# Performance work log

Hardware: AMD Instinct MI355X
Metric: run time of the kernel (lower is better)

## Reference

```python
import jax, jax.numpy as jnp
import numpy as np

V = 6890          # SMPL vertex count
RAYS, POINTS = 256, 64
LATENT_DIM = 16
RES_HI, RES_LO = 10, 4


def posenc(x, res):
    # NeRF-style encoding: [x, sin(2^k x), cos(2^k x)] for k in 0..res-1 -> D*(1+2*res)
    freqs = 2.0 ** jnp.arange(res, dtype=x.dtype)            # [res]
    xf = x[..., None, :] * freqs[:, None]                    # [..., res, D]
    n = x.shape[:-1]
    s = jnp.sin(xf).reshape(*n, -1)
    c = jnp.cos(xf).reshape(*n, -1)
    return jnp.concatenate([x, s, c], axis=-1)


def setup_inputs() -> dict:
    key = jax.random.key(0)
    ks = jax.random.split(key, 12)
    inp = {}
    inp['pts'] = jax.random.normal(ks[0], (RAYS, POINTS, 6), jnp.float32)
    inp['keypoints'] = jax.random.normal(ks[1], (V, 3), jnp.float32)
    # invertible per-vertex 4x4 transforms: identity + small noise, stored [4,4,V]
    noise = 0.1 * jax.random.normal(ks[2], (4, 4, V), jnp.float32)
    inp['trans_kp'] = jnp.eye(4, dtype=jnp.float32)[:, :, None] + noise
    inp['neighbors'] = jax.random.randint(ks[3], (V, 7), 0, V, jnp.int32)
    inp['rest_pose'] = jax.random.normal(ks[4], (V, 3), jnp.float32)
    inp['latent'] = jax.random.normal(ks[5], (V, LATENT_DIM), jnp.float32)
    d_in = 7 * ((2 * RES_HI + 1) * 4 + LATENT_DIM)  # 700
    inp['W1'] = 0.05 * jax.random.normal(ks[6], (d_in, 256), jnp.float32)
    inp['b1'] = jnp.zeros((256,), jnp.float32)
    inp['W2'] = 0.05 * jax.random.normal(ks[7], (256, 256), jnp.float32)
    inp['b2'] = jnp.zeros((256,), jnp.float32)
    inp['W3'] = 0.05 * jax.random.normal(ks[8], (256, 256), jnp.float32)
    inp['b3'] = jnp.zeros((256,), jnp.float32)
    return inp


def reference(pts, keypoints, trans_kp, neighbors, rest_pose, latent,
              W1, b1, W2, b2, W3, b3):
    rays, points, _ = pts.shape
    p, view_dir = jnp.split(pts, 2, axis=-1)
    p = p.reshape(rays * points, 3)                          # [N,3]

    # brute-force 1-NN of p into keypoints
    d2 = ((p * p).sum(-1, keepdims=True)
          - 2.0 * p @ keypoints.T
          + (keypoints * keypoints).sum(-1))                 # [N,V]
    knn_index = jnp.argmin(d2, axis=1)                       # [N]

    # inverse transforms, keep rotation part: [3,3,V]
    T = jnp.linalg.inv(jnp.transpose(trans_kp, (2, 0, 1)))   # [V,4,4]
    R = jnp.transpose(T, (1, 2, 0))[:3, :3]                  # [3,3,V]

    vidx = neighbors[knn_index]                              # [N,7]
    vdist = p[:, None, :] - keypoints[vidx]                  # [N,7,3]

    diff = p - keypoints[knn_index]                          # [N,3]
    Rg = R[:, :, knn_index]                                  # [3,3,N]
    direction = jnp.einsum('ijn,nj->ni', Rg, diff)           # [N,3]
    nrm = jnp.linalg.norm(direction, axis=-1, keepdims=True)
    direction = direction / jnp.maximum(nrm, 1e-12)

    vfeat = jnp.concatenate(
        [rest_pose[vidx].reshape(-1, 21),
         jnp.linalg.norm(vdist, axis=-1)], axis=-1)          # [N,28]
    lfeat = latent[vidx].reshape(-1, 7 * latent.shape[1])    # [N,112]

    h = jnp.concatenate([posenc(vfeat, RES_HI), lfeat], -1)  # [N,700]
    h = jax.nn.relu(h @ W1 + b1)
    h = jax.nn.relu(h @ W2 + b2)
    h = h @ W3 + b3                                          # [N,256]

    out = jnp.concatenate([h, posenc(direction, RES_LO)], -1)  # [N,283]
    return out.reshape(rays, points, -1)
```

## Files before the change

### kernel.cpp

```cpp
#include <hip/hip_runtime.h>
#include <hip/hip_bf16.h>
#include <math.h>

#define V_N   6890
#define N_PTS 16384
#define D_IN  700
#define D_INP 704
#define D_HID 256
#define D_OUT 283
#define NCHUNK 32
#define CHUNK  216
#define GAP_EPS 1e-4f

#define RINV4_OFF 0
#define KP4_OFF   82688
#define RP4_OFF   110272
#define PB4_OFF   170640
#define WT1_OFF   2267792
#define WT2_OFF   2357904
#define WT3_OFF   2390672
#define X_OFF     2423440

typedef __attribute__((ext_vector_type(8))) short short8;
typedef __attribute__((ext_vector_type(4))) float f32x4;

__device__ __forceinline__ unsigned short f2bf(float f) {
    unsigned int u = __builtin_bit_cast(unsigned int, f);
    u += 0x7fffu + ((u >> 16) & 1u);
    return (unsigned short)(u >> 16);
}

__device__ __forceinline__ float fsin(float x) {
    return __builtin_amdgcn_sinf(__builtin_amdgcn_fractf(x * 0.15915494309189535f));
}
__device__ __forceinline__ float fcos(float x) {
    return __builtin_amdgcn_cosf(__builtin_amdgcn_fractf(x * 0.15915494309189535f));
}

__device__ __forceinline__ void glds16(const void* g, void* l) {
    __builtin_amdgcn_global_load_lds(
        (const __attribute__((address_space(1))) void*)g,
        (__attribute__((address_space(3))) void*)l, 16, 0, 0);
}

__device__ __forceinline__ int swzoff(int r, int sub) {
    return ((r << 2) | (sub ^ ((r >> 1) & 3))) << 4;
}

__device__ __forceinline__ int rescan64(const float* __restrict__ pts,
                                        const float4* __restrict__ kp4,
                                        int nn, int lane) {
    double pxd = (double)pts[nn*6+0], pyd = (double)pts[nn*6+1], pzd = (double)pts[nn*6+2];
    double ppd = pxd*pxd + pyd*pyd + pzd*pzd;
    double best = 1e300; int bbi = 0x7fffffff;
    for (int jj = lane; jj < V_N; jj += 64) {
        float4 k = kp4[jj];
        double kx = (double)k.x, ky = (double)k.y, kz = (double)k.z;
        double d = ppd - 2.0*(pxd*kx + pyd*ky + pzd*kz) + (kx*kx + ky*ky + kz*kz);
        if (d < best || (d == best && jj < bbi)) { best = d; bbi = jj; }
    }
#pragma unroll
    for (int off = 32; off >= 1; off >>= 1) {
        double od = __shfl_xor(best, off);
        int    oi = __shfl_xor(bbi, off);
        if (od < best || (od == best && oi < bbi)) { best = od; bbi = oi; }
    }
    return bbi;
}

#define SCAN_BLOCKS 2048
#define PREP_BLOCKS 27
__global__ __launch_bounds__(256) void prep_scan_kernel(
    const float* __restrict__ pts, const float* __restrict__ keyp,
    const float* __restrict__ trans, const float* __restrict__ restp,
    const float* __restrict__ W1, const float* __restrict__ W2,
    const float* __restrict__ W3,
    float4* __restrict__ rinv4, float4* __restrict__ kp4, float4* __restrict__ rp4,
    unsigned short* __restrict__ wt1, unsigned short* __restrict__ wt2,
    unsigned short* __restrict__ wt3, float4* __restrict__ pb4)
{
    __shared__ float4 s_kp[CHUNK];
    int bx = blockIdx.x, tid = threadIdx.x;

    if (bx < SCAN_BLOCKS) {
        int c = bx >> 6;
        int n = (bx & 63) * 256 + tid;
        int v0 = c * CHUNK;
        int nv = min(V_N - v0, CHUNK);
        if (tid < nv) {
            int v = v0 + tid;
            float kx = keyp[v*3+0], ky = keyp[v*3+1], kz = keyp[v*3+2];
            s_kp[tid] = make_float4(kx, ky, kz, kx*kx + ky*ky + kz*kz);
        }
        __syncthreads();

        float px2n = -2.0f * pts[n*6+0], py2n = -2.0f * pts[n*6+1], pz2n = -2.0f * pts[n*6+2];
        float m1 = 1e30f, m2 = 1e30f;
        int bi = 0x7fffffff;

#define KNN_STEP(kk, jj)                                                    \
    {                                                                       \
        float d = __builtin_fmaf(px2n, kk.x,                                \
                  __builtin_fmaf(py2n, kk.y,                                \
                  __builtin_fmaf(pz2n, kk.z, kk.w)));                       \
        bool lt = d < m1;                                                   \
        bi = lt ? (jj) : bi;                                                \
        m2 = __builtin_amdgcn_fmed3f(m1, m2, d);                            \
        m1 = fminf(m1, d);                                                  \
    }
        int j = 0;
        for (; j + 8 <= nv; j += 8) {
            float4 k0 = s_kp[j],   k1 = s_kp[j+1], k2 = s_kp[j+2], k3 = s_kp[j+3];
            float4 k4 = s_kp[j+4], k5 = s_kp[j+5], k6 = s_kp[j+6], k7 = s_kp[j+7];
            KNN_STEP(k0, v0+j);   KNN_STEP(k1, v0+j+1);
            KNN_STEP(k2, v0+j+2); KNN_STEP(k3, v0+j+3);
            KNN_STEP(k4, v0+j+4); KNN_STEP(k5, v0+j+5);
            KNN_STEP(k6, v0+j+6); KNN_STEP(k7, v0+j+7);
        }
        for (; j < nv; ++j) {
            float4 k0 = s_kp[j];
            KNN_STEP(k0, v0+j);
        }
#undef KNN_STEP
        pb4[(size_t)n * NCHUNK + c] = make_float4(m1, m2, __int_as_float(bi), 0.0f);

    } else if (bx < SCAN_BLOCKS + PREP_BLOCKS) {
        int v = (bx - SCAN_BLOCKS) * 256 + tid;
        if (v >= V_N) return;
        float m[16];
#pragma unroll
        for (int i = 0; i < 16; ++i) m[i] = trans[i * V_N + v];

        float i0  =  m[5]*m[10]*m[15] - m[5]*m[11]*m[14] - m[9]*m[6]*m[15] + m[9]*m[7]*m[14] + m[13]*m[6]*m[11] - m[13]*m[7]*m[10];
        float i4  = -m[4]*m[10]*m[15] + m[4]*m[11]*m[14] + m[8]*m[6]*m[15] - m[8]*m[7]*m[14] - m[12]*m[6]*m[11] + m[12]*m[7]*m[10];
        float i8  =  m[4]*m[9]*m[15]  - m[4]*m[11]*m[13] - m[8]*m[5]*m[15] + m[8]*m[7]*m[13] + m[12]*m[5]*m[11] - m[12]*m[7]*m[9];
        float i12 = -m[4]*m[9]*m[14]  + m[4]*m[10]*m[13] + m[8]*m[5]*m[14] - m[8]*m[6]*m[13] - m[12]*m[5]*m[10] + m[12]*m[6]*m[9];
        float i1  = -m[1]*m[10]*m[15] + m[1]*m[11]*m[14] + m[9]*m[2]*m[15] - m[9]*m[3]*m[14] - m[13]*m[2]*m[11] + m[13]*m[3]*m[10];
        float i5  =  m[0]*m[10]*m[15] - m[0]*m[11]*m[14] - m[8]*m[2]*m[15] + m[8]*m[3]*m[14] + m[12]*m[2]*m[11] - m[12]*m[3]*m[10];
        float i9  = -m[0]*m[9]*m[15]  + m[0]*m[11]*m[13] + m[8]*m[1]*m[15] - m[8]*m[3]*m[13] - m[12]*m[1]*m[11] + m[12]*m[3]*m[9];
        float i2  =  m[1]*m[6]*m[15]  - m[1]*m[7]*m[14]  - m[5]*m[2]*m[15] + m[5]*m[3]*m[14] + m[13]*m[2]*m[7]  - m[13]*m[3]*m[6];
        float i6  = -m[0]*m[6]*m[15]  + m[0]*m[7]*m[14]  + m[4]*m[2]*m[15] - m[4]*m[3]*m[14] - m[12]*m[2]*m[7]  + m[12]*m[3]*m[6];
        float i10 =  m[0]*m[5]*m[15]  - m[0]*m[7]*m[13]  - m[4]*m[1]*m[15] + m[4]*m[3]*m[13] + m[12]*m[1]*m[7]  - m[12]*m[3]*m[5];

        float det = m[0]*i0 + m[1]*i4 + m[2]*i8 + m[3]*i12;
        float id = 1.0f / det;
        rinv4[v*3+0] = make_float4(i0*id, i1*id, i2*id, i4*id);
        rinv4[v*3+1] = make_float4(i5*id, i6*id, i8*id, i9*id);
        rinv4[v*3+2] = make_float4(i10*id, 0.0f, 0.0f, 0.0f);

        float kx = keyp[v*3], ky = keyp[v*3+1], kz = keyp[v*3+2];
        kp4[v] = make_float4(kx, ky, kz, kx*kx + ky*ky + kz*kz);
        rp4[v] = make_float4(restp[v*3], restp[v*3+1], restp[v*3+2], 0.0f);
    } else {
        int idx = (bx - SCAN_BLOCKS - PREP_BLOCKS) * 256 + tid;
        const int N1 = 256 * D_INP;
        const int N2 = 256 * 256;
        if (idx < N1) {
            int n = idx / D_INP, k = idx - n * D_INP;
            float v = (k < D_IN) ? W1[k * 256 + n] : 0.0f;
            wt1[n * D_INP + k] = f2bf(v);
        } else if (idx < N1 + N2) {
            int t = idx - N1;
            int n = t >> 8, k = t & 255;
            wt2[n * 256 + k] = f2bf(W2[k * 256 + n]);
        } else if (idx < N1 + 2 * N2) {
            int t = idx - N1 - N2;
            int n = t >> 8, k = t & 255;
            wt3[n * 256 + k] = f2bf(W3[k * 256 + n]);
        }
    }
}

__global__ __launch_bounds__(256) void feat_kernel(
    const float* __restrict__ pts, const int* __restrict__ neigh,
    const float* __restrict__ latent, const float4* __restrict__ rinv4,
    const float4* __restrict__ kp4, const float4* __restrict__ rp4,
    const float4* __restrict__ pb4, unsigned short* __restrict__ X,
    float* __restrict__ out)
{
    __shared__ float s_vf[4][2][29];
    __shared__ float s_dir[4][2][4];

    int t = threadIdx.x;
    int w = t >> 6, lane = t & 63;
    int n0 = blockIdx.x * 8 + w * 2;
    int ph = lane >> 5, g = lane & 31;

    float pxA = pts[n0*6+0],     pyA = pts[n0*6+1],     pzA = pts[n0*6+2];
    float pxB = pts[(n0+1)*6+0], pyB = pts[(n0+1)*6+1], pzB = pts[(n0+1)*6+2];

    float4 P = pb4[(size_t)(n0 + ph) * NCHUNK + g];
    float m1 = P.x, m2 = P.y;
    int   bi = __float_as_int(P.z);
#pragma unroll
    for (int off = 1; off <= 16; off <<= 1) {
        float o1 = __shfl_xor(m1, off);
        float o2 = __shfl_xor(m2, off);
        int   ob = __shfl_xor(bi, off);
        float nm2 = fminf(fminf(m2, o2), fmaxf(m1, o1));
        bool take = (o1 < m1) || (o1 == m1 && ob < bi);
        bi = take ? ob : bi;
        m1 = fminf(m1, o1);
        m2 = nm2;
    }
    unsigned long long ambmask = __ballot(m2 - m1 < GAP_EPS);
    if (ambmask & 1ull) {
        int r = rescan64(pts, kp4, n0, lane);
        if (ph == 0) bi = r;
    }
    if (ambmask & (1ull << 32)) {
        int r = rescan64(pts, kp4, n0 + 1, lane);
        if (ph == 1) bi = r;
    }

    int p = ph, j = g;
    int k8 = bi;
    float px = p ? pxB : pxA, py = p ? pyB : pyA, pz = p ? pzB : pzA;

    int v7 = 0;
    if (j < 7) {
        v7 = neigh[k8*7 + j];
        float4 kq = kp4[v7];
        float4 rq = rp4[v7];
        float dx = px - kq.x, dy = py - kq.y, dz = pz - kq.z;
        s_vf[w][p][j*3+0] = rq.x;
        s_vf[w][p][j*3+1] = rq.y;
        s_vf[w][p][j*3+2] = rq.z;
        s_vf[w][p][21+j]  = sqrtf(dx*dx + dy*dy + dz*dz);
    } else if (j == 7) {
        float4 kq = kp4[k8];
        float ddx = px - kq.x, ddy = py - kq.y, ddz = pz - kq.z;
        float4 R0 = rinv4[k8*3+0];
        float4 R1 = rinv4[k8*3+1];
        float4 R2 = rinv4[k8*3+2];
        float d0 = R0.x*ddx + R0.y*ddy + R0.z*ddz;
        float d1 = R0.w*ddx + R1.x*ddy + R1.y*ddz;
        float d2 = R1.z*ddx + R1.w*ddy + R2.x*ddz;
        float nrm = fmaxf(sqrtf(d0*d0 + d1*d1 + d2*d2), 1e-12f);
        s_dir[w][p][0] = d0/nrm; s_dir[w][p][1] = d1/nrm; s_dir[w][p][2] = d2/nrm;
    }

#pragma unroll
    for (int pp = 0; pp < 2; ++pp) {
        int n = n0 + pp;
        float dir0 = s_dir[w][pp][0];
        float dir1 = s_dir[w][pp][1];
        float dir2 = s_dir[w][pp][2];

        if (lane < 27) {
            float val;
            if (lane < 3) {
                val = (lane == 0) ? dir0 : (lane == 1) ? dir1 : dir2;
            } else {
                int tt = (lane < 15) ? lane - 3 : lane - 15;
                int m = tt % 3;
                float db = (m == 0) ? dir0 : (m == 1) ? dir1 : dir2;
                float a = db * (float)(1 << (tt/3));
                val = (lane < 15) ? fsin(a) : fcos(a);
            }
            out[(size_t)n*D_OUT + 256 + lane] = val;
        }

#pragma unroll
        for (int it = 0; it < 3; ++it) {
            int base = it * 256 + (lane << 2);
            bool in_range = base < D_INP;
            int region = (base < 28) ? 0 : (base < 308) ? 1 : (base < 588) ? 2
                       : (base < 700) ? 3 : 4;

            int t0 = (region == 1) ? base - 28 : (region == 2) ? base - 308 : 0;
            int q = t0 / 28;
            int r = t0 - q * 28;
            float f0 = (float)(1 << q);
            float a[4];
#pragma unroll
            for (int jj = 0; jj < 4; ++jj) {
                int rj; float fj;
                if (region == 0) { rj = base + jj; fj = 1.0f; }
                else if (region <= 2) {
                    rj = r + jj; fj = f0;
                    if (rj >= 28) { rj -= 28; fj = f0 * 2.0f; }
                } else { rj = 0; fj = 0.0f; }
                a[jj] = s_vf[w][pp][rj] * fj;
            }
            int idxc = (region == 3) ? (base - 588) >> 4 : 0;
            int vL = __shfl(v7, pp*32 + idxc);

            unsigned short r0, r1, r2, r3;
            if (region == 0) {
                r0 = f2bf(a[0]); r1 = f2bf(a[1]); r2 = f2bf(a[2]); r3 = f2bf(a[3]);
            } else if (region == 1) {
                r0 = f2bf(fsin(a[0])); r1 = f2bf(fsin(a[1]));
                r2 = f2bf(fsin(a[2])); r3 = f2bf(fsin(a[3]));
            } else if (region == 2) {
                r0 = f2bf(fcos(a[0])); r1 = f2bf(fcos(a[1]));
                r2 = f2bf(fcos(a[2])); r3 = f2bf(fcos(a[3]));
            } else if (region == 3) {
                int t3 = base - 588;
                float4 lv = *(const float4*)&latent[vL * 16 + (t3 & 15)];
                r0 = f2bf(lv.x); r1 = f2bf(lv.y); r2 = f2bf(lv.z); r3 = f2bf(lv.w);
            } else {
                r0 = r1 = r2 = r3 = 0;
            }
            if (in_range)
                *(ushort4*)&X[(size_t)n * D_INP + base] = make_ushort4(r0, r1, r2, r3);
        }
    }
}

#define HLD 264
__global__ __launch_bounds__(512) void mlp_kernel(
    const unsigned short* __restrict__ X,
    const unsigned short* __restrict__ wt1,
    const unsigned short* __restrict__ wt2,
    const unsigned short* __restrict__ wt3,
    const float* __restrict__ b1, const float* __restrict__ b2,
    const float* __restrict__ b3, float* __restrict__ out)
{
    __shared__ unsigned short As[2][64 * 32];
    __shared__ unsigned short Ws[2][256 * 32];
    __shared__ unsigned short H1[64 * HLD];
    __shared__ unsigned short H2[64 * HLD];

    int t = threadIdx.x, l = t & 63, w = t >> 6;
    int bm = blockIdx.x * 64;
    int mbase = (w >> 2) * 32, nbase = (w & 3) * 64;
    int lrow = l & 15, lk = (l >> 4) * 8, sub = l >> 4;
    int col0 = l & 15, rquad = (l >> 4) * 4;

    f32x4 acc[2][4];
    short8 af[2], bf[4];

    auto stageA = [&](int buf, int k0) {
        if (t < 256) {
            int r = t >> 2, sg = (t & 3) ^ ((r >> 1) & 3);
            glds16(X + (size_t)(bm + r) * D_INP + k0 + sg * 8,
                   (char*)As[buf] + t * 16);
        }
    };
    auto stageW = [&](int buf, const unsigned short* wsrc, int ld, int k0) {
#pragma unroll
        for (int i = 0; i < 2; ++i) {
            int c = i * 512 + t;
            int r = c >> 2, sg = (c & 3) ^ ((r >> 1) & 3);
            glds16(wsrc + (size_t)r * ld + k0 + sg * 8,
                   (char*)Ws[buf] + (size_t)c * 16);
        }
    };

#pragma unroll
    for (int mi = 0; mi < 2; ++mi)
#pragma unroll
        for (int ni = 0; ni < 4; ++ni) acc[mi][ni] = {0.f, 0.f, 0.f, 0.f};

    stageA(0, 0);
    stageW(0, wt1, D_INP, 0);
    __syncthreads();
    const int NK1 = D_INP / 32;
    for (int ks = 0; ks < NK1; ++ks) {
        int cur = ks & 1;
        if (ks + 1 < NK1) {
            stageA(cur ^ 1, (ks + 1) * 32);
            stageW(cur ^ 1, wt1, D_INP, (ks + 1) * 32);
        }
#pragma unroll
        for (int mi = 0; mi < 2; ++mi)
            af[mi] = *(const short8*)((const char*)As[cur] + swzoff(mbase + mi*16 + lrow, sub));
#pragma unroll
        for (int ni = 0; ni < 4; ++ni)
            bf[ni] = *(const short8*)((const char*)Ws[cur] + swzoff(nbase + ni*16 + lrow, sub));
#pragma unroll
        for (int mi = 0; mi < 2; ++mi)
#pragma unroll
            for (int ni = 0; ni < 4; ++ni)
                acc[mi][ni] = __builtin_amdgcn_mfma_f32_16x16x32_bf16(
                    af[mi], bf[ni], acc[mi][ni], 0, 0, 0);
        __syncthreads();
    }
    stageW(0, wt2, D_HID, 0);
#pragma unroll
    for (int mi = 0; mi < 2; ++mi)
#pragma unroll
        for (int ni = 0; ni < 4; ++ni) {
            int col = nbase + ni * 16 + col0;
            float bv = b1[col];
#pragma unroll
            for (int r = 0; r < 4; ++r) {
                int row = mbase + mi * 16 + rquad + r;
                H1[row * HLD + col] = f2bf(fmaxf(acc[mi][ni][r] + bv, 0.0f));
            }
        }
    __syncthreads();

#pragma unroll
    for (int mi = 0; mi < 2; ++mi)
#pragma unroll
        for (int ni = 0; ni < 4; ++ni) acc[mi][ni] = {0.f, 0.f, 0.f, 0.f};

    const int NK2 = D_HID / 32;
    for (int ks = 0; ks < NK2; ++ks) {
        int cur = ks & 1;
        if (ks + 1 < NK2) stageW(cur ^ 1, wt2, D_HID, (ks + 1) * 32);
#pragma unroll
        for (int mi = 0; mi < 2; ++mi)
            af[mi] = *(const short8*)&H1[(mbase + mi * 16 + lrow) * HLD + ks * 32 + lk];
#pragma unroll
        for (int ni = 0; ni < 4; ++ni)
            bf[ni] = *(const short8*)((const char*)Ws[cur] + swzoff(nbase + ni*16 + lrow, sub));
#pragma unroll
        for (int mi = 0; mi < 2; ++mi)
#pragma unroll
            for (int ni = 0; ni < 4; ++ni)
                acc[mi][ni] = __builtin_amdgcn_mfma_f32_16x16x32_bf16(
                    af[mi], bf[ni], acc[mi][ni], 0, 0, 0);
        __syncthreads();
    }
    stageW(0, wt3, D_HID, 0);
#pragma unroll
    for (int mi = 0; mi < 2; ++mi)
#pragma unroll
        for (int ni = 0; ni < 4; ++ni) {
            int col = nbase + ni * 16 + col0;
            float bv = b2[col];
#pragma unroll
            for (int r = 0; r < 4; ++r) {
                int row = mbase + mi * 16 + rquad + r;
                H2[row * HLD + col] = f2bf(fmaxf(acc[mi][ni][r] + bv, 0.0f));
            }
        }
    __syncthreads();

#pragma unroll
    for (int mi = 0; mi < 2; ++mi)
#pragma unroll
        for (int ni = 0; ni < 4; ++ni) acc[mi][ni] = {0.f, 0.f, 0.f, 0.f};

    for (int ks = 0; ks < NK2; ++ks) {
        int cur = ks & 1;
        if (ks + 1 < NK2) stageW(cur ^ 1, wt3, D_HID, (ks + 1) * 32);
#pragma unroll
        for (int mi = 0; mi < 2; ++mi)
            af[mi] = *(const short8*)&H2[(mbase + mi * 16 + lrow) * HLD + ks * 32 + lk];
#pragma unroll
        for (int ni = 0; ni < 4; ++ni)
            bf[ni] = *(const short8*)((const char*)Ws[cur] + swzoff(nbase + ni*16 + lrow, sub));
#pragma unroll
        for (int mi = 0; mi < 2; ++mi)
#pragma unroll
            for (int ni = 0; ni < 4; ++ni)
                acc[mi][ni] = __builtin_amdgcn_mfma_f32_16x16x32_bf16(
                    af[mi], bf[ni], acc[mi][ni], 0, 0, 0);
        __syncthreads();
    }
#pragma unroll
    for (int mi = 0; mi < 2; ++mi)
#pragma unroll
        for (int ni = 0; ni < 4; ++ni) {
            int col = nbase + ni * 16 + col0;
            float bv = b3[col];
#pragma unroll
            for (int r = 0; r < 4; ++r) {
                int row = bm + mbase + mi * 16 + rquad + r;
                out[(size_t)row * D_OUT + col] = acc[mi][ni][r] + bv;
            }
        }
}

extern "C" void kernel_launch(void* const* d_in, const int* in_sizes, int n_in,
                              void* d_out, int out_size, void* d_ws, size_t ws_size,
                              hipStream_t stream) {
    const float* pts    = (const float*)d_in[0];
    const float* keyp   = (const float*)d_in[1];
    const float* trans  = (const float*)d_in[2];
    const int*   neigh  = (const int*)d_in[3];
    const float* restp  = (const float*)d_in[4];
    const float* latent = (const float*)d_in[5];
    const float* W1     = (const float*)d_in[6];
    const float* b1     = (const float*)d_in[7];
    const float* W2     = (const float*)d_in[8];
    const float* b2     = (const float*)d_in[9];
    const float* W3     = (const float*)d_in[10];
    const float* b3     = (const float*)d_in[11];
    float* out = (float*)d_out;

    float* wsf = (float*)d_ws;
    float4*         rinv4 = (float4*)(wsf + RINV4_OFF);
    float4*         kp4   = (float4*)(wsf + KP4_OFF);
    float4*         rp4   = (float4*)(wsf + RP4_OFF);
    float4*         pb4   = (float4*)(wsf + PB4_OFF);
    unsigned short* wt1   = (unsigned short*)(wsf + WT1_OFF);
    unsigned short* wt2   = (unsigned short*)(wsf + WT2_OFF);
    unsigned short* wt3   = (unsigned short*)(wsf + WT3_OFF);
    unsigned short* X     = (unsigned short*)(wsf + X_OFF);

    int wconv_blocks = (256*D_INP + 2*256*256 + 255) / 256;
    prep_scan_kernel<<<SCAN_BLOCKS + PREP_BLOCKS + wconv_blocks, 256, 0, stream>>>(
        pts, keyp, trans, restp, W1, W2, W3, rinv4, kp4, rp4, wt1, wt2, wt3, pb4);
    feat_kernel<<<N_PTS/8, 256, 0, stream>>>(pts, neigh, latent, rinv4,
                                             kp4, rp4, pb4, X, out);
    mlp_kernel<<<N_PTS/64, 512, 0, stream>>>(X, wt1, wt2, wt3, b1, b2, b3, out);
}
```

Before: 173.9 us.

## Split KNN resolve and exact double-precision rescan into dedicated kernels with compaction

Moves the per-point merge of chunk partial minima out of feat_kernel into a separate resolve kernel. Points whose best and second-best distances are nearly tied are appended to a compacted list through an atomic counter. A separate exact kernel then load-balances the double-precision rescans across all waves. This removes divergent rescans that stalled whole feat_kernel waves, at the cost of two extra kernel launches and a round trip through global memory for the knn indices.

```diff
diff --git a/kernel.cpp b/kernel.cpp
--- a/kernel.cpp
+++ b/kernel.cpp
@@ -15,6 +15,9 @@
 #define RINV4_OFF 0
 #define KP4_OFF   82688
 #define RP4_OFF   110272
+#define KNN_OFF   137856
+#define CNT_OFF   154240
+#define FLAG_OFF  154256
 #define PB4_OFF   170640
 #define WT1_OFF   2267792
 #define WT2_OFF   2357904
@@ -45,27 +48,6 @@
 
 __device__ __forceinline__ int swzoff(int r, int sub) {
     return ((r << 2) | (sub ^ ((r >> 1) & 3))) << 4;
-}
-
-__device__ __forceinline__ int rescan64(const float* __restrict__ pts,
-                                        const float4* __restrict__ kp4,
-                                        int nn, int lane) {
-    double pxd = (double)pts[nn*6+0], pyd = (double)pts[nn*6+1], pzd = (double)pts[nn*6+2];
-    double ppd = pxd*pxd + pyd*pyd + pzd*pzd;
-    double best = 1e300; int bbi = 0x7fffffff;
-    for (int jj = lane; jj < V_N; jj += 64) {
-        float4 k = kp4[jj];
-        double kx = (double)k.x, ky = (double)k.y, kz = (double)k.z;
-        double d = ppd - 2.0*(pxd*kx + pyd*ky + pzd*kz) + (kx*kx + ky*ky + kz*kz);
-        if (d < best || (d == best && jj < bbi)) { best = d; bbi = jj; }
-    }
-#pragma unroll
-    for (int off = 32; off >= 1; off >>= 1) {
-        double od = __shfl_xor(best, off);
-        int    oi = __shfl_xor(bbi, off);
-        if (od < best || (od == best && oi < bbi)) { best = od; bbi = oi; }
-    }
-    return bbi;
 }
 
 #define SCAN_BLOCKS 2048
@@ -77,10 +59,12 @@
     const float* __restrict__ W3,
     float4* __restrict__ rinv4, float4* __restrict__ kp4, float4* __restrict__ rp4,
     unsigned short* __restrict__ wt1, unsigned short* __restrict__ wt2,
-    unsigned short* __restrict__ wt3, float4* __restrict__ pb4)
+    unsigned short* __restrict__ wt3, float4* __restrict__ pb4,
+    int* __restrict__ cnt)
 {
     __shared__ float4 s_kp[CHUNK];
     int bx = blockIdx.x, tid = threadIdx.x;
+    if (bx == 0 && tid == 0) cnt[0] = 0;
 
     if (bx < SCAN_BLOCKS) {
         int c = bx >> 6;
@@ -171,11 +155,92 @@
     }
 }
 
+__global__ __launch_bounds__(256) void knn_resolve_kernel(
+    const float4* __restrict__ pb4, int* __restrict__ knn,
+    int* __restrict__ cnt, int* __restrict__ flag_list)
+{
+    int t = threadIdx.x;
+    int pl = t >> 3, sub = t & 7;
+    int n = blockIdx.x * 32 + pl;
+
+    const float4* base = pb4 + (size_t)n * NCHUNK + sub * 4;
+    float4 P0 = base[0], P1 = base[1], P2 = base[2], P3 = base[3];
+
+    float m1 = P0.x, m2 = P0.y;
+    int   bi = __float_as_int(P0.z);
+#define PMERGE(P)                                                       \
+    {                                                                   \
+        float om1 = P.x, om2 = P.y;  int ob = __float_as_int(P.z);      \
+        float nm2 = fminf(fminf(m2, om2), fmaxf(m1, om1));              \
+        bool take = (om1 < m1) || (om1 == m1 && ob < bi);               \
+        bi = take ? ob : bi;  m1 = fminf(m1, om1);  m2 = nm2;           \
+    }
+    PMERGE(P1); PMERGE(P2); PMERGE(P3);
+#undef PMERGE
+#pragma unroll
+    for (int off = 1; off <= 4; off <<= 1) {
+        float om1 = __shfl_xor(m1, off);
+        float om2 = __shfl_xor(m2, off);
+        int   ob  = __shfl_xor(bi, off);
+        float nm2 = fminf(fminf(m2, om2), fmaxf(m1, om1));
+        bool take = (om1 < m1) || (om1 == m1 && ob < bi);
+        bi = take ? ob : bi;  m1 = fminf(m1, om1);  m2 = nm2;
+    }
+    if (sub == 0) {
+        knn[n] = bi;
+        if (m2 - m1 < GAP_EPS) {
+            int s = atomicAdd(cnt, 1);
+            flag_list[s] = n;
+        }
+    }
+}
+
+__global__ __launch_bounds__(256) void knn_exact_kernel(
+    const float* __restrict__ pts, const float4* __restrict__ kp4,
+    const int* __restrict__ cnt, const int* __restrict__ flag_list,
+    int* __restrict__ knn)
+{
+    int lane = threadIdx.x & 63;
+    int gwave = (blockIdx.x * 256 + threadIdx.x) >> 6;
+    int nwaves = gridDim.x * 4;
+    int total = cnt[0];
+
+    for (int it = gwave; it < total; it += nwaves) {
+        int nn = flag_list[it];
+        double pxd = (double)pts[nn*6+0], pyd = (double)pts[nn*6+1], pzd = (double)pts[nn*6+2];
+        double ppd = pxd*pxd + pyd*pyd + pzd*pzd;
+        double best = 1e300; int bbi = 0x7fffffff;
+        for (int b = lane; b < 6912; b += 256) {
+            int j0 = b, j1 = b + 64, j2 = b + 128, j3 = b + 192;
+            float4 k0 = kp4[min(j0, V_N-1)];
+            float4 k1 = kp4[min(j1, V_N-1)];
+            float4 k2 = kp4[min(j2, V_N-1)];
+            float4 k3 = kp4[min(j3, V_N-1)];
+#define EVAL(kk, jj)                                                          \
+            if (jj < V_N) {                                                   \
+                double kx = (double)kk.x, ky = (double)kk.y, kz = (double)kk.z;\
+                double d = ppd - 2.0*(pxd*kx + pyd*ky + pzd*kz)               \
+                         + (kx*kx + ky*ky + kz*kz);                           \
+                if (d < best || (d == best && jj < bbi)) { best = d; bbi = jj; }\
+            }
+            EVAL(k0, j0); EVAL(k1, j1); EVAL(k2, j2); EVAL(k3, j3);
+#undef EVAL
+        }
+#pragma unroll
+        for (int off = 32; off >= 1; off >>= 1) {
+            double od = __shfl_xor(best, off);
+            int    oi = __shfl_xor(bbi, off);
+            if (od < best || (od == best && oi < bbi)) { best = od; bbi = oi; }
+        }
+        if (lane == 0) knn[nn] = bbi;
+    }
+}
+
 __global__ __launch_bounds__(256) void feat_kernel(
     const float* __restrict__ pts, const int* __restrict__ neigh,
     const float* __restrict__ latent, const float4* __restrict__ rinv4,
     const float4* __restrict__ kp4, const float4* __restrict__ rp4,
-    const float4* __restrict__ pb4, unsigned short* __restrict__ X,
+    const int* __restrict__ knn, unsigned short* __restrict__ X,
     float* __restrict__ out)
 {
     __shared__ float s_vf[4][2][29];
@@ -184,38 +249,11 @@
     int t = threadIdx.x;
     int w = t >> 6, lane = t & 63;
     int n0 = blockIdx.x * 8 + w * 2;
-    int ph = lane >> 5, g = lane & 31;
-
-    float pxA = pts[n0*6+0],     pyA = pts[n0*6+1],     pzA = pts[n0*6+2];
-    float pxB = pts[(n0+1)*6+0], pyB = pts[(n0+1)*6+1], pzB = pts[(n0+1)*6+2];
-
-    float4 P = pb4[(size_t)(n0 + ph) * NCHUNK + g];
-    float m1 = P.x, m2 = P.y;
-    int   bi = __float_as_int(P.z);
-#pragma unroll
-    for (int off = 1; off <= 16; off <<= 1) {
-        float o1 = __shfl_xor(m1, off);
-        float o2 = __shfl_xor(m2, off);
-        int   ob = __shfl_xor(bi, off);
-        float nm2 = fminf(fminf(m2, o2), fmaxf(m1, o1));
-        bool take = (o1 < m1) || (o1 == m1 && ob < bi);
-        bi = take ? ob : bi;
-        m1 = fminf(m1, o1);
-        m2 = nm2;
-    }
-    unsigned long long ambmask = __ballot(m2 - m1 < GAP_EPS);
-    if (ambmask & 1ull) {
-        int r = rescan64(pts, kp4, n0, lane);
-        if (ph == 0) bi = r;
-    }
-    if (ambmask & (1ull << 32)) {
-        int r = rescan64(pts, kp4, n0 + 1, lane);
-        if (ph == 1) bi = r;
-    }
-
-    int p = ph, j = g;
-    int k8 = bi;
-    float px = p ? pxB : pxA, py = p ? pyB : pyA, pz = p ? pzB : pzA;
+
+    int p = lane >> 5, j = lane & 31;
+    int np = n0 + p;
+    int k8 = knn[np];
+    float px = pts[np*6+0], py = pts[np*6+1], pz = pts[np*6+2];
 
     int v7 = 0;
     if (j < 7) {
@@ -487,6 +525,9 @@
     float4*         rinv4 = (float4*)(wsf + RINV4_OFF);
     float4*         kp4   = (float4*)(wsf + KP4_OFF);
     float4*         rp4   = (float4*)(wsf + RP4_OFF);
+    int*            knn   = (int*)(wsf + KNN_OFF);
+    int*            cnt   = (int*)(wsf + CNT_OFF);
+    int*            flg   = (int*)(wsf + FLAG_OFF);
     float4*         pb4   = (float4*)(wsf + PB4_OFF);
     unsigned short* wt1   = (unsigned short*)(wsf + WT1_OFF);
     unsigned short* wt2   = (unsigned short*)(wsf + WT2_OFF);
@@ -495,8 +536,11 @@
 
     int wconv_blocks = (256*D_INP + 2*256*256 + 255) / 256;
     prep_scan_kernel<<<SCAN_BLOCKS + PREP_BLOCKS + wconv_blocks, 256, 0, stream>>>(
-        pts, keyp, trans, restp, W1, W2, W3, rinv4, kp4, rp4, wt1, wt2, wt3, pb4);
+        pts, keyp, trans, restp, W1, W2, W3, rinv4, kp4, rp4, wt1, wt2, wt3,
+        pb4, cnt);
+    knn_resolve_kernel<<<N_PTS/32, 256, 0, stream>>>(pb4, knn, cnt, flg);
+    knn_exact_kernel<<<256, 256, 0, stream>>>(pts, kp4, cnt, flg, knn);
     feat_kernel<<<N_PTS/8, 256, 0, stream>>>(pts, neigh, latent, rinv4,
-                                             kp4, rp4, pb4, X, out);
+                                             kp4, rp4, knn, X, out);
     mlp_kernel<<<N_PTS/64, 512, 0, stream>>>(X, wt1, wt2, wt3, b1, b2, b3, out);
 }
```

New measurement: 177.5 us. 2.1% more time.

## Register-block KNN scan over two points, shrink MLP row tile, unroll rescan

Applied to the files above, without the earlier changes.

The KNN scan now has each thread handle two query points per keypoint chunk. This halves the scan block count and reuses each LDS keypoint load across two distance evaluations. The MLP kernel shrinks its row tile from 64 to 32 rows, with all 8 waves splitting the 256 output columns. That doubles the block count for better CU occupancy, but each block reloads the full weight set, so weight staging traffic per row doubles. The double-precision rescan fallback is unrolled by four with clamped loads to add memory-level parallelism.

```diff
diff --git a/kernel.cpp b/kernel.cpp
--- a/kernel.cpp
+++ b/kernel.cpp
@@ -53,11 +53,21 @@
     double pxd = (double)pts[nn*6+0], pyd = (double)pts[nn*6+1], pzd = (double)pts[nn*6+2];
     double ppd = pxd*pxd + pyd*pyd + pzd*pzd;
     double best = 1e300; int bbi = 0x7fffffff;
-    for (int jj = lane; jj < V_N; jj += 64) {
-        float4 k = kp4[jj];
-        double kx = (double)k.x, ky = (double)k.y, kz = (double)k.z;
-        double d = ppd - 2.0*(pxd*kx + pyd*ky + pzd*kz) + (kx*kx + ky*ky + kz*kz);
-        if (d < best || (d == best && jj < bbi)) { best = d; bbi = jj; }
+    for (int b = lane; b < 6912; b += 256) {
+        int j0 = b, j1 = b + 64, j2 = b + 128, j3 = b + 192;
+        float4 k0 = kp4[min(j0, V_N-1)];
+        float4 k1 = kp4[min(j1, V_N-1)];
+        float4 k2 = kp4[min(j2, V_N-1)];
+        float4 k3 = kp4[min(j3, V_N-1)];
+#define EVAL(kk, jj)                                                          \
+        if (jj < V_N) {                                                       \
+            double kx = (double)kk.x, ky = (double)kk.y, kz = (double)kk.z;   \
+            double d = ppd - 2.0*(pxd*kx + pyd*ky + pzd*kz)                   \
+                     + (kx*kx + ky*ky + kz*kz);                               \
+            if (d < best || (d == best && jj < bbi)) { best = d; bbi = jj; }  \
+        }
+        EVAL(k0, j0); EVAL(k1, j1); EVAL(k2, j2); EVAL(k3, j3);
+#undef EVAL
     }
 #pragma unroll
     for (int off = 32; off >= 1; off >>= 1) {
@@ -68,7 +78,7 @@
     return bbi;
 }
 
-#define SCAN_BLOCKS 2048
+#define SCAN_BLOCKS 1024
 #define PREP_BLOCKS 27
 __global__ __launch_bounds__(256) void prep_scan_kernel(
     const float* __restrict__ pts, const float* __restrict__ keyp,
@@ -83,8 +93,10 @@
     int bx = blockIdx.x, tid = threadIdx.x;
 
     if (bx < SCAN_BLOCKS) {
-        int c = bx >> 6;
-        int n = (bx & 63) * 256 + tid;
+        int g = bx & 31;
+        int c = bx >> 5;
+        int nA = g * 512 + tid;
+        int nB = nA + 256;
         int v0 = c * CHUNK;
         int nv = min(V_N - v0, CHUNK);
         if (tid < nv) {
@@ -94,19 +106,27 @@
         }
         __syncthreads();
 
-        float px2n = -2.0f * pts[n*6+0], py2n = -2.0f * pts[n*6+1], pz2n = -2.0f * pts[n*6+2];
-        float m1 = 1e30f, m2 = 1e30f;
-        int bi = 0x7fffffff;
+        float pxA2n = -2.0f * pts[nA*6+0], pyA2n = -2.0f * pts[nA*6+1], pzA2n = -2.0f * pts[nA*6+2];
+        float pxB2n = -2.0f * pts[nB*6+0], pyB2n = -2.0f * pts[nB*6+1], pzB2n = -2.0f * pts[nB*6+2];
+        float m1A = 1e30f, m2A = 1e30f; int biA = 0x7fffffff;
+        float m1B = 1e30f, m2B = 1e30f; int biB = 0x7fffffff;
 
 #define KNN_STEP(kk, jj)                                                    \
     {                                                                       \
-        float d = __builtin_fmaf(px2n, kk.x,                                \
-                  __builtin_fmaf(py2n, kk.y,                                \
-                  __builtin_fmaf(pz2n, kk.z, kk.w)));                       \
-        bool lt = d < m1;                                                   \
-        bi = lt ? (jj) : bi;                                                \
-        m2 = __builtin_amdgcn_fmed3f(m1, m2, d);                            \
-        m1 = fminf(m1, d);                                                  \
+        float dA = __builtin_fmaf(pxA2n, kk.x,                              \
+                   __builtin_fmaf(pyA2n, kk.y,                              \
+                   __builtin_fmaf(pzA2n, kk.z, kk.w)));                     \
+        float dB = __builtin_fmaf(pxB2n, kk.x,                              \
+                   __builtin_fmaf(pyB2n, kk.y,                              \
+                   __builtin_fmaf(pzB2n, kk.z, kk.w)));                     \
+        bool ltA = dA < m1A;                                                \
+        biA = ltA ? (jj) : biA;                                             \
+        m2A = __builtin_amdgcn_fmed3f(m1A, m2A, dA);                        \
+        m1A = fminf(m1A, dA);                                               \
+        bool ltB = dB < m1B;                                                \
+        biB = ltB ? (jj) : biB;                                             \
+        m2B = __builtin_amdgcn_fmed3f(m1B, m2B, dB);                        \
+        m1B = fminf(m1B, dB);                                               \
     }
         int j = 0;
         for (; j + 8 <= nv; j += 8) {
@@ -122,7 +142,8 @@
             KNN_STEP(k0, v0+j);
         }
 #undef KNN_STEP
-        pb4[(size_t)n * NCHUNK + c] = make_float4(m1, m2, __int_as_float(bi), 0.0f);
+        pb4[(size_t)nA * NCHUNK + c] = make_float4(m1A, m2A, __int_as_float(biA), 0.0f);
+        pb4[(size_t)nB * NCHUNK + c] = make_float4(m1B, m2B, __int_as_float(biB), 0.0f);
 
     } else if (bx < SCAN_BLOCKS + PREP_BLOCKS) {
         int v = (bx - SCAN_BLOCKS) * 256 + tid;
@@ -317,22 +338,22 @@
     const float* __restrict__ b1, const float* __restrict__ b2,
     const float* __restrict__ b3, float* __restrict__ out)
 {
-    __shared__ unsigned short As[2][64 * 32];
+    __shared__ unsigned short As[2][32 * 32];
     __shared__ unsigned short Ws[2][256 * 32];
-    __shared__ unsigned short H1[64 * HLD];
-    __shared__ unsigned short H2[64 * HLD];
+    __shared__ unsigned short H1[32 * HLD];
+    __shared__ unsigned short H2[32 * HLD];
 
     int t = threadIdx.x, l = t & 63, w = t >> 6;
-    int bm = blockIdx.x * 64;
-    int mbase = (w >> 2) * 32, nbase = (w & 3) * 64;
+    int bm = blockIdx.x * 32;
+    int nbase = w * 32;
     int lrow = l & 15, lk = (l >> 4) * 8, sub = l >> 4;
     int col0 = l & 15, rquad = (l >> 4) * 4;
 
-    f32x4 acc[2][4];
-    short8 af[2], bf[4];
+    f32x4 acc[2][2];
+    short8 af[2], bf[2];
 
     auto stageA = [&](int buf, int k0) {
-        if (t < 256) {
+        if (t < 128) {
             int r = t >> 2, sg = (t & 3) ^ ((r >> 1) & 3);
             glds16(X + (size_t)(bm + r) * D_INP + k0 + sg * 8,
                    (char*)As[buf] + t * 16);
@@ -351,7 +372,7 @@
 #pragma unroll
     for (int mi = 0; mi < 2; ++mi)
 #pragma unroll
-        for (int ni = 0; ni < 4; ++ni) acc[mi][ni] = {0.f, 0.f, 0.f, 0.f};
+        for (int ni = 0; ni < 2; ++ni) acc[mi][ni] = {0.f, 0.f, 0.f, 0.f};
 
     stageA(0, 0);
     stageW(0, wt1, D_INP, 0);
@@ -365,14 +386,14 @@
         }
 #pragma unroll
         for (int mi = 0; mi < 2; ++mi)
-            af[mi] = *(const short8*)((const char*)As[cur] + swzoff(mbase + mi*16 + lrow, sub));
-#pragma unroll
-        for (int ni = 0; ni < 4; ++ni)
+            af[mi] = *(const short8*)((const char*)As[cur] + swzoff(mi*16 + lrow, sub));
+#pragma unroll
+        for (int ni = 0; ni < 2; ++ni)
             bf[ni] = *(const short8*)((const char*)Ws[cur] + swzoff(nbase + ni*16 + lrow, sub));
 #pragma unroll
         for (int mi = 0; mi < 2; ++mi)
 #pragma unroll
-            for (int ni = 0; ni < 4; ++ni)
+            for (int ni = 0; ni < 2; ++ni)
                 acc[mi][ni] = __builtin_amdgcn_mfma_f32_16x16x32_bf16(
                     af[mi], bf[ni], acc[mi][ni], 0, 0, 0);
         __syncthreads();
@@ -381,12 +402,12 @@
 #pragma unroll
     for (int mi = 0; mi < 2; ++mi)
 #pragma unroll
-        for (int ni = 0; ni < 4; ++ni) {
+        for (int ni = 0; ni < 2; ++ni) {
             int col = nbase + ni * 16 + col0;
             float bv = b1[col];
 #pragma unroll
             for (int r = 0; r < 4; ++r) {
-                int row = mbase + mi * 16 + rquad + r;
+                int row = mi * 16 + rquad + r;
                 H1[row * HLD + col] = f2bf(fmaxf(acc[mi][ni][r] + bv, 0.0f));
             }
         }
@@ -395,7 +416,7 @@
 #pragma unroll
     for (int mi = 0; mi < 2; ++mi)
 #pragma unroll
-        for (int ni = 0; ni < 4; ++ni) acc[mi][ni] = {0.f, 0.f, 0.f, 0.f};
+        for (int ni = 0; ni < 2; ++ni) acc[mi][ni] = {0.f, 0.f, 0.f, 0.f};
 
     const int NK2 = D_HID / 32;
     for (int ks = 0; ks < NK2; ++ks) {
@@ -403,14 +424,14 @@
         if (ks + 1 < NK2) stageW(cur ^ 1, wt2, D_HID, (ks + 1) * 32);
 #pragma unroll
         for (int mi = 0; mi < 2; ++mi)
-            af[mi] = *(const short8*)&H1[(mbase + mi * 16 + lrow) * HLD + ks * 32 + lk];
-#pragma unroll
-        for (int ni = 0; ni < 4; ++ni)
+            af[mi] = *(const short8*)&H1[(mi * 16 + lrow) * HLD + ks * 32 + lk];
+#pragma unroll
+        for (int ni = 0; ni < 2; ++ni)
             bf[ni] = *(const short8*)((const char*)Ws[cur] + swzoff(nbase + ni*16 + lrow, sub));
 #pragma unroll
         for (int mi = 0; mi < 2; ++mi)
 #pragma unroll
-            for (int ni = 0; ni < 4; ++ni)
+            for (int ni = 0; ni < 2; ++ni)
                 acc[mi][ni] = __builtin_amdgcn_mfma_f32_16x16x32_bf16(
                     af[mi], bf[ni], acc[mi][ni], 0, 0, 0);
         __syncthreads();
@@ -419,12 +440,12 @@
 #pragma unroll
     for (int mi = 0; mi < 2; ++mi)
 #pragma unroll
-        for (int ni = 0; ni < 4; ++ni) {
+        for (int ni = 0; ni < 2; ++ni) {
             int col = nbase + ni * 16 + col0;
             float bv = b2[col];
 #pragma unroll
             for (int r = 0; r < 4; ++r) {
-                int row = mbase + mi * 16 + rquad + r;
+                int row = mi * 16 + rquad + r;
                 H2[row * HLD + col] = f2bf(fmaxf(acc[mi][ni][r] + bv, 0.0f));
             }
         }
@@ -433,21 +454,21 @@
 #pragma unroll
     for (int mi = 0; mi < 2; ++mi)
 #pragma unroll
-        for (int ni = 0; ni < 4; ++ni) acc[mi][ni] = {0.f, 0.f, 0.f, 0.f};
+        for (int ni = 0; ni < 2; ++ni) acc[mi][ni] = {0.f, 0.f, 0.f, 0.f};
 
     for (int ks = 0; ks < NK2; ++ks) {
         int cur = ks & 1;
         if (ks + 1 < NK2) stageW(cur ^ 1, wt3, D_HID, (ks + 1) * 32);
 #pragma unroll
         for (int mi = 0; mi < 2; ++mi)
-            af[mi] = *(const short8*)&H2[(mbase + mi * 16 + lrow) * HLD + ks * 32 + lk];
-#pragma unroll
-        for (int ni = 0; ni < 4; ++ni)
+            af[mi] = *(const short8*)&H2[(mi * 16 + lrow) * HLD + ks * 32 + lk];
+#pragma unroll
+        for (int ni = 0; ni < 2; ++ni)
             bf[ni] = *(const short8*)((const char*)Ws[cur] + swzoff(nbase + ni*16 + lrow, sub));
 #pragma unroll
         for (int mi = 0; mi < 2; ++mi)
 #pragma unroll
-            for (int ni = 0; ni < 4; ++ni)
+            for (int ni = 0; ni < 2; ++ni)
                 acc[mi][ni] = __builtin_amdgcn_mfma_f32_16x16x32_bf16(
                     af[mi], bf[ni], acc[mi][ni], 0, 0, 0);
         __syncthreads();
@@ -455,12 +476,12 @@
 #pragma unroll
     for (int mi = 0; mi < 2; ++mi)
 #pragma unroll
-        for (int ni = 0; ni < 4; ++ni) {
+        for (int ni = 0; ni < 2; ++ni) {
             int col = nbase + ni * 16 + col0;
             float bv = b3[col];
 #pragma unroll
             for (int r = 0; r < 4; ++r) {
-                int row = bm + mbase + mi * 16 + rquad + r;
+                int row = bm + mi * 16 + rquad + r;
                 out[(size_t)row * D_OUT + col] = acc[mi][ni][r] + bv;
             }
         }
@@ -498,5 +519,5 @@
         pts, keyp, trans, restp, W1, W2, W3, rinv4, kp4, rp4, wt1, wt2, wt3, pb4);
     feat_kernel<<<N_PTS/8, 256, 0, stream>>>(pts, neigh, latent, rinv4,
                                              kp4, rp4, pb4, X, out);
-    mlp_kernel<<<N_PTS/64, 512, 0, stream>>>(X, wt1, wt2, wt3, b1, b2, b3, out);
-}
+    mlp_kernel<<<N_PTS/32, 512, 0, stream>>>(X, wt1, wt2, wt3, b1, b2, b3, out);
+}
```

New measurement: 161.7 us. 7.0% less time.
